# Optimization experiments

Measured on AMD Instinct MI355X. Metric: run time of the kernel, lower is better.

## Reference

```python
import jax, jax.numpy as jnp
import numpy as np

N, NS, D, HID = 8192, 512, 1024, 1024  # nodes, num_edges, f_dim, mlp hidden (max(f_dim,128))


def layernorm(x, g, b, eps=1e-5):
    m = x.mean(-1, keepdims=True)
    v = x.var(-1, keepdims=True)
    return (x - m) / jnp.sqrt(v + eps) * g + b


def mask_topk(a, kk):
    # keep only the top-kk entries of each row (vectorized version of mask_attn)
    _, idx = jax.lax.top_k(a, kk)
    rows = jnp.arange(a.shape[0])[:, None]
    mask = jnp.zeros(a.shape, a.dtype).at[rows, idx].set(1.0)
    return a * mask


def setup_inputs() -> dict:
    key = jax.random.key(0)
    ks = jax.random.split(key, 16)
    xavier = lambda k, i, o: jax.random.uniform(k, (i, o), jnp.float32, -1.0, 1.0) * np.sqrt(6.0 / (i + o))
    return {
        "inputs": jax.random.normal(ks[0], (N, D), jnp.float32),
        "noise": jax.random.normal(ks[1], (NS, D), jnp.float32),
        "edges_mu": jax.random.normal(ks[2], (1, D), jnp.float32),
        "edges_logsigma": xavier(ks[3], 1, D),
        "Wq": xavier(ks[4], D, D), "bq": jnp.zeros((D,), jnp.float32),
        "Wk": xavier(ks[5], D, D), "bk": jnp.zeros((D,), jnp.float32),
        "Wv": xavier(ks[6], D, D), "bv": jnp.zeros((D,), jnp.float32),
        "W1": xavier(ks[7], 2 * D, HID), "b1": jnp.zeros((HID,), jnp.float32),
        "W2": xavier(ks[8], HID, D), "b2": jnp.zeros((D,), jnp.float32),
        "g_in": jnp.ones((D,), jnp.float32), "b_in": jnp.zeros((D,), jnp.float32),
        "g_e": jnp.ones((D,), jnp.float32), "b_e": jnp.zeros((D,), jnp.float32),
        "k_n": 64,
        "k_e": 8,
    }


def reference(inputs, noise, edges_mu, edges_logsigma, Wq, bq, Wk, bk, Wv, bv,
              W1, b1, W2, b2, g_in, b_in, g_e, b_e, k_n, k_e):
    n, d = inputs.shape
    scale = d ** -0.5
    eps = 1e-8
    x = layernorm(inputs, g_in, b_in)                       # norm_input
    k = jax.nn.relu(x @ Wk + bk)                            # [N, D]
    v = jax.nn.relu(x @ Wv + bv)                            # [N, D]
    edges = edges_mu + jnp.exp(edges_logsigma) * noise      # [NS, D]
    # single iteration (iters=1)
    edges = layernorm(edges, g_e, b_e)                      # norm_edgs
    q = jax.nn.relu(edges @ Wq + bq)                        # [NS, D]
    dots = jnp.einsum('ni,mi->nm', q, k) * scale            # [NS, N]
    attn = jax.nn.softmax(dots, axis=1) + eps
    attn = attn / attn.sum(axis=1, keepdims=True)
    attn = mask_topk(attn, k_n)
    updates = jnp.einsum('nm,md->nd', attn, v)              # [NS, D]
    edges = jnp.concatenate([edges, updates], axis=1)       # [NS, 2D]
    edges = jax.nn.relu(edges @ W1 + b1) @ W2 + b2          # mlp -> [NS, D]
    q2 = x @ Wq + bq                                        # no relu in source
    k2 = jax.nn.relu(edges @ Wk + bk)                       # [NS, D]
    dots_v = jnp.einsum('ni,mi->nm', q2, k2) * scale        # [N, NS]
    attn_v = jax.nn.softmax(dots_v, axis=1)
    H = mask_topk(attn_v, k_e)
    return edges, H, dots
```

## Files before the change

kernel.cpp:

```cpp
#include <hip/hip_runtime.h>
#include <stdint.h>
#include <stddef.h>

typedef unsigned short u16;
typedef __bf16 bf16x8 __attribute__((ext_vector_type(8)));
typedef float f32x4 __attribute__((ext_vector_type(4)));

#define DEV __device__ __forceinline__

DEV float bf2f(u16 u){ union{uint32_t i; float f;} c; c.i=(uint32_t)u<<16; return c.f; }
DEV u16 f2bf(float f){ union{float f; uint32_t i;} c; c.f=f; uint32_t x=c.i;
  uint32_t r = x + 0x7FFFu + ((x>>16)&1u); return (u16)(r>>16); }
DEV uint32_t fmap(float f){ union{float f; uint32_t u;} c; c.f=f;
  return (c.u & 0x80000000u) ? ~c.u : (c.u | 0x80000000u); }
DEV float funmap(uint32_t u){ union{uint32_t u; float f;} c;
  c.u = (u & 0x80000000u) ? (u & 0x7FFFFFFFu) : ~u; return c.f; }
DEV void split2(float x, u16& h, u16& l){ h = f2bf(x); l = f2bf(x - bf2f(h)); }

DEV void xcd_swizzle(int& bx, int& by){
  const int gx = gridDim.x, nwg = gx * gridDim.y;
  const int b  = blockIdx.x + gx*blockIdx.y;
  const int sb = (b & 7)*(nwg >> 3) + (b >> 3);
  bx = sb % gx; by = sb / gx;
}

DEV float bredsum(float v, float* buf, int tid){
  #pragma unroll
  for(int o=32;o;o>>=1) v += __shfl_down(v,o);
  __syncthreads();
  if((tid&63)==0) buf[tid>>6]=v;
  __syncthreads();
  return buf[0]+buf[1]+buf[2]+buf[3];
}
DEV float bredmax(float v, float* buf, int tid){
  #pragma unroll
  for(int o=32;o;o>>=1) v = fmaxf(v, __shfl_down(v,o));
  __syncthreads();
  if((tid&63)==0) buf[tid>>6]=v;
  __syncthreads();
  return fmaxf(fmaxf(buf[0],buf[1]),fmaxf(buf[2],buf[3]));
}
DEV int bredsumi(int v, int* buf, int tid){
  #pragma unroll
  for(int o=32;o;o>>=1) v += __shfl_down(v,o);
  __syncthreads();
  if((tid&63)==0) buf[tid>>6]=v;
  __syncthreads();
  return buf[0]+buf[1]+buf[2]+buf[3];
}

template<bool RELU, int SK>
__global__ __launch_bounds__(256)
void gemm1_64(const u16* __restrict__ A, int lda,
              const u16* __restrict__ Bt, int ldb,
              const float* __restrict__ bias, float scale,
              u16* __restrict__ outb, float* __restrict__ outf,
              float* __restrict__ part,
              int K, int ldc, int M)
{
  __shared__ __align__(16) u16 As[64*32];
  __shared__ __align__(16) u16 Bs[128*32];
  const int tid = threadIdx.x, lane = tid&63, wave = tid>>6;
  const int m0 = blockIdx.y*64, n0 = blockIdx.x*128;
  const int wm = (wave>>1)*32, wn = (wave&1)*64;
  const int ml = lane&15, quad = lane>>4;
  const int ks = K / SK;
  const int kbeg = blockIdx.z * ks;
  const u16* pa  = A  + (size_t)(m0+(tid>>2))*lda + kbeg + (tid&3)*8;
  const u16* pb0 = Bt + (size_t)(n0+(tid>>2))*ldb + kbeg + (tid&3)*8;
  const u16* pb1 = Bt + (size_t)(n0+64+(tid>>2))*ldb + kbeg + (tid&3)*8;

  f32x4 acc[2][4];
  #pragma unroll
  for(int i=0;i<2;i++)
    #pragma unroll
    for(int j=0;j<4;j++) acc[i][j] = (f32x4){0.f,0.f,0.f,0.f};

  uint4 ra=*(const uint4*)pa, rb0=*(const uint4*)pb0, rb1=*(const uint4*)pb1;
  for(int k0=0;k0<ks;k0+=32){
    __syncthreads();
    *(uint4*)&As[tid*8]       = ra;
    *(uint4*)&Bs[tid*8]       = rb0;
    *(uint4*)&Bs[(256+tid)*8] = rb1;
    __syncthreads();
    if(k0+32<ks){
      ra  = *(const uint4*)(pa +k0+32);
      rb0 = *(const uint4*)(pb0+k0+32);
      rb1 = *(const uint4*)(pb1+k0+32);
    }
    bf16x8 af[2], bf[4];
    #pragma unroll
    for(int mi=0;mi<2;mi++) af[mi] = *(const bf16x8*)&As[(wm+mi*16+ml)*32 + quad*8];
    #pragma unroll
    for(int ni=0;ni<4;ni++) bf[ni] = *(const bf16x8*)&Bs[(wn+ni*16+ml)*32 + quad*8];
    #pragma unroll
    for(int mi=0;mi<2;mi++)
      #pragma unroll
      for(int ni=0;ni<4;ni++)
        acc[mi][ni] = __builtin_amdgcn_mfma_f32_16x16x32_bf16(af[mi], bf[ni], acc[mi][ni], 0,0,0);
  }
  #pragma unroll
  for(int mi=0;mi<2;mi++){
    const int rbase = m0 + wm + mi*16 + quad*4;
    #pragma unroll
    for(int ni=0;ni<4;ni++){
      const int col = n0 + wn + ni*16 + ml;
      if(SK==1){
        const float bv = bias ? bias[col] : 0.f;
        #pragma unroll
        for(int r=0;r<4;r++){
          float v = acc[mi][ni][r]*scale + bv;
          if(RELU) v = fmaxf(v, 0.f);
          const size_t idx = (size_t)(rbase + r)*ldc + col;
          if(outb) outb[idx] = f2bf(v);
          if(outf) outf[idx] = v;
        }
      }else{
        #pragma unroll
        for(int r=0;r<4;r++)
          part[((size_t)blockIdx.z*M + rbase + r)*ldc + col] = acc[mi][ni][r];
      }
    }
  }
}

template<bool RELU>
__global__ __launch_bounds__(256)
void gemm1_128(const u16* __restrict__ A, int lda,
               const u16* __restrict__ Bt, int ldb,
               const float* __restrict__ bias, float scale,
               u16* __restrict__ outb, float* __restrict__ outf,
               int K, int ldc)
{
  __shared__ __align__(16) u16 As[128*32];
  __shared__ __align__(16) u16 Bs[128*32];
  const int tid = threadIdx.x, lane = tid&63, wave = tid>>6;
  int bxs, bys; xcd_swizzle(bxs, bys);
  const int m0 = bys*128, n0 = bxs*128;
  const int wm = (wave>>1)*64, wn = (wave&1)*64;
  const int ml = lane&15, quad = lane>>4;
  const u16* pa0 = A  + (size_t)(m0+(tid>>2))*lda    + (tid&3)*8;
  const u16* pa1 = A  + (size_t)(m0+64+(tid>>2))*lda + (tid&3)*8;
  const u16* pb0 = Bt + (size_t)(n0+(tid>>2))*ldb    + (tid&3)*8;
  const u16* pb1 = Bt + (size_t)(n0+64+(tid>>2))*ldb + (tid&3)*8;

  f32x4 acc[4][4];
  #pragma unroll
  for(int i=0;i<4;i++)
    #pragma unroll
    for(int j=0;j<4;j++) acc[i][j] = (f32x4){0.f,0.f,0.f,0.f};

  uint4 ra0=*(const uint4*)pa0, ra1=*(const uint4*)pa1;
  uint4 rb0=*(const uint4*)pb0, rb1=*(const uint4*)pb1;
  for(int k0=0;k0<K;k0+=32){
    __syncthreads();
    *(uint4*)&As[tid*8]       = ra0;
    *(uint4*)&As[(256+tid)*8] = ra1;
    *(uint4*)&Bs[tid*8]       = rb0;
    *(uint4*)&Bs[(256+tid)*8] = rb1;
    __syncthreads();
    if(k0+32<K){
      ra0 = *(const uint4*)(pa0+k0+32);
      ra1 = *(const uint4*)(pa1+k0+32);
      rb0 = *(const uint4*)(pb0+k0+32);
      rb1 = *(const uint4*)(pb1+k0+32);
    }
    bf16x8 af[4], bf[4];
    #pragma unroll
    for(int mi=0;mi<4;mi++) af[mi] = *(const bf16x8*)&As[(wm+mi*16+ml)*32 + quad*8];
    #pragma unroll
    for(int ni=0;ni<4;ni++) bf[ni] = *(const bf16x8*)&Bs[(wn+ni*16+ml)*32 + quad*8];
    #pragma unroll
    for(int mi=0;mi<4;mi++)
      #pragma unroll
      for(int ni=0;ni<4;ni++)
        acc[mi][ni] = __builtin_amdgcn_mfma_f32_16x16x32_bf16(af[mi], bf[ni], acc[mi][ni], 0,0,0);
  }
  #pragma unroll
  for(int mi=0;mi<4;mi++){
    const int rbase = m0 + wm + mi*16 + quad*4;
    #pragma unroll
    for(int ni=0;ni<4;ni++){
      const int col = n0 + wn + ni*16 + ml;
      const float bv = bias ? bias[col] : 0.f;
      #pragma unroll
      for(int r=0;r<4;r++){
        float v = acc[mi][ni][r]*scale + bv;
        if(RELU) v = fmaxf(v, 0.f);
        const size_t idx = (size_t)(rbase + r)*ldc + col;
        if(outb) outb[idx] = f2bf(v);
        if(outf) outf[idx] = v;
      }
    }
  }
}

__global__ __launch_bounds__(256)
void gemm_kv_128(const u16* __restrict__ A, int lda,
                 const u16* __restrict__ Bt, int ldb,
                 const float* __restrict__ bk, const float* __restrict__ bv,
                 u16* __restrict__ kb, u16* __restrict__ vb, int K)
{
  __shared__ __align__(16) u16 As[128*32];
  __shared__ __align__(16) u16 Bs[128*32];
  const int tid = threadIdx.x, lane = tid&63, wave = tid>>6;
  int bxs, bys; xcd_swizzle(bxs, bys);
  const int m0 = bys*128, n0 = bxs*128;
  const int wm = (wave>>1)*64, wn = (wave&1)*64;
  const int ml = lane&15, quad = lane>>4;
  const u16* pa0 = A  + (size_t)(m0+(tid>>2))*lda    + (tid&3)*8;
  const u16* pa1 = A  + (size_t)(m0+64+(tid>>2))*lda + (tid&3)*8;
  const u16* pb0 = Bt + (size_t)(n0+(tid>>2))*ldb    + (tid&3)*8;
  const u16* pb1 = Bt + (size_t)(n0+64+(tid>>2))*ldb + (tid&3)*8;

  f32x4 acc[4][4];
  #pragma unroll
  for(int i=0;i<4;i++)
    #pragma unroll
    for(int j=0;j<4;j++) acc[i][j] = (f32x4){0.f,0.f,0.f,0.f};

  uint4 ra0=*(const uint4*)pa0, ra1=*(const uint4*)pa1;
  uint4 rb0=*(const uint4*)pb0, rb1=*(const uint4*)pb1;
  for(int k0=0;k0<K;k0+=32){
    __syncthreads();
    *(uint4*)&As[tid*8]       = ra0;
    *(uint4*)&As[(256+tid)*8] = ra1;
    *(uint4*)&Bs[tid*8]       = rb0;
    *(uint4*)&Bs[(256+tid)*8] = rb1;
    __syncthreads();
    if(k0+32<K){
      ra0 = *(const uint4*)(pa0+k0+32);
      ra1 = *(const uint4*)(pa1+k0+32);
      rb0 = *(const uint4*)(pb0+k0+32);
      rb1 = *(const uint4*)(pb1+k0+32);
    }
    bf16x8 af[4], bf[4];
    #pragma unroll
    for(int mi=0;mi<4;mi++) af[mi] = *(const bf16x8*)&As[(wm+mi*16+ml)*32 + quad*8];
    #pragma unroll
    for(int ni=0;ni<4;ni++) bf[ni] = *(const bf16x8*)&Bs[(wn+ni*16+ml)*32 + quad*8];
    #pragma unroll
    for(int mi=0;mi<4;mi++)
      #pragma unroll
      for(int ni=0;ni<4;ni++)
        acc[mi][ni] = __builtin_amdgcn_mfma_f32_16x16x32_bf16(af[mi], bf[ni], acc[mi][ni], 0,0,0);
  }
  #pragma unroll
  for(int mi=0;mi<4;mi++){
    const int rbase = m0 + wm + mi*16 + quad*4;
    #pragma unroll
    for(int ni=0;ni<4;ni++){
      const int col = n0 + wn + ni*16 + ml;
      const bool isv = col >= 1024;
      const int c2 = col & 1023;
      const float bb = isv ? bv[c2] : bk[c2];
      u16* outp = isv ? vb : kb;
      #pragma unroll
      for(int r=0;r<4;r++){
        const float v = fmaxf(acc[mi][ni][r] + bb, 0.f);
        outp[(size_t)(rbase + r)*1024 + c2] = f2bf(v);
      }
    }
  }
}

template<bool RELU, int SK>
__global__ __launch_bounds__(256)
void gemm3_64(const u16* __restrict__ Ah, const u16* __restrict__ Al, int lda,
              const u16* __restrict__ Bh, const u16* __restrict__ Bl, int ldb,
              const float* __restrict__ bias, float scale,
              u16* __restrict__ outh, u16* __restrict__ outl,
              float* __restrict__ outf, float* __restrict__ part,
              int K, int ldc, int M)
{
  __shared__ __align__(16) u16 AsH[64*32];
  __shared__ __align__(16) u16 AsL[64*32];
  __shared__ __align__(16) u16 BsH[128*32];
  __shared__ __align__(16) u16 BsL[128*32];
  const int tid = threadIdx.x, lane = tid&63, wave = tid>>6;
  const int m0 = blockIdx.y*64, n0 = blockIdx.x*128;
  const int wm = (wave>>1)*32, wn = (wave&1)*64;
  const int ml = lane&15, quad = lane>>4;
  const int ks = K / SK;
  const int kbeg = blockIdx.z * ks;
  const size_t ao  = (size_t)(m0+(tid>>2))*lda + kbeg + (tid&3)*8;
  const size_t bo0 = (size_t)(n0+(tid>>2))*ldb + kbeg + (tid&3)*8;
  const size_t bo1 = (size_t)(n0+64+(tid>>2))*ldb + kbeg + (tid&3)*8;

  f32x4 acc[2][4];
  #pragma unroll
  for(int i=0;i<2;i++)
    #pragma unroll
    for(int j=0;j<4;j++) acc[i][j] = (f32x4){0.f,0.f,0.f,0.f};

  uint4 rah=*(const uint4*)(Ah+ao),  ral=*(const uint4*)(Al+ao);
  uint4 rbh0=*(const uint4*)(Bh+bo0), rbl0=*(const uint4*)(Bl+bo0);
  uint4 rbh1=*(const uint4*)(Bh+bo1), rbl1=*(const uint4*)(Bl+bo1);
  for(int k0=0;k0<ks;k0+=32){
    __syncthreads();
    *(uint4*)&AsH[tid*8]       = rah;
    *(uint4*)&AsL[tid*8]       = ral;
    *(uint4*)&BsH[tid*8]       = rbh0;
    *(uint4*)&BsL[tid*8]       = rbl0;
    *(uint4*)&BsH[(256+tid)*8] = rbh1;
    *(uint4*)&BsL[(256+tid)*8] = rbl1;
    __syncthreads();
    if(k0+32<ks){
      const int s = k0+32;
      rah =*(const uint4*)(Ah+ao +s); ral =*(const uint4*)(Al+ao +s);
      rbh0=*(const uint4*)(Bh+bo0+s); rbl0=*(const uint4*)(Bl+bo0+s);
      rbh1=*(const uint4*)(Bh+bo1+s); rbl1=*(const uint4*)(Bl+bo1+s);
    }
    bf16x8 afh[2], afl[2], bfh[4], bfl[4];
    #pragma unroll
    for(int mi=0;mi<2;mi++){
      const int o = (wm+mi*16+ml)*32 + quad*8;
      afh[mi] = *(const bf16x8*)&AsH[o];
      afl[mi] = *(const bf16x8*)&AsL[o];
    }
    #pragma unroll
    for(int ni=0;ni<4;ni++){
      const int o = (wn+ni*16+ml)*32 + quad*8;
      bfh[ni] = *(const bf16x8*)&BsH[o];
      bfl[ni] = *(const bf16x8*)&BsL[o];
    }
    #pragma unroll
    for(int mi=0;mi<2;mi++)
      #pragma unroll
      for(int ni=0;ni<4;ni++){
        acc[mi][ni] = __builtin_amdgcn_mfma_f32_16x16x32_bf16(afh[mi], bfh[ni], acc[mi][ni], 0,0,0);
        acc[mi][ni] = __builtin_amdgcn_mfma_f32_16x16x32_bf16(afh[mi], bfl[ni], acc[mi][ni], 0,0,0);
        acc[mi][ni] = __builtin_amdgcn_mfma_f32_16x16x32_bf16(afl[mi], bfh[ni], acc[mi][ni], 0,0,0);
      }
  }
  #pragma unroll
  for(int mi=0;mi<2;mi++){
    const int rbase = m0 + wm + mi*16 + quad*4;
    #pragma unroll
    for(int ni=0;ni<4;ni++){
      const int col = n0 + wn + ni*16 + ml;
      if(SK==1){
        const float bv = bias ? bias[col] : 0.f;
        #pragma unroll
        for(int r=0;r<4;r++){
          float v = acc[mi][ni][r]*scale + bv;
          if(RELU) v = fmaxf(v, 0.f);
          const size_t idx = (size_t)(rbase + r)*ldc + col;
          if(outh){ u16 h, l; split2(v, h, l); outh[idx] = h; outl[idx] = l; }
          if(outf) outf[idx] = v;
        }
      }else{
        #pragma unroll
        for(int r=0;r<4;r++)
          part[((size_t)blockIdx.z*M + rbase + r)*ldc + col] = acc[mi][ni][r];
      }
    }
  }
}

__global__ __launch_bounds__(256)
void gemm3_128(const u16* __restrict__ Ah, const u16* __restrict__ Al, int lda,
               const u16* __restrict__ Bh, const u16* __restrict__ Bl, int ldb,
               const float* __restrict__ bias, float scale,
               float* __restrict__ outf, int K, int ldc)
{
  __shared__ __align__(16) u16 AsH[128*32];
  __shared__ __align__(16) u16 AsL[128*32];
  __shared__ __align__(16) u16 BsH[128*32];
  __shared__ __align__(16) u16 BsL[128*32];
  const int tid = threadIdx.x, lane = tid&63, wave = tid>>6;
  int bxs, bys; xcd_swizzle(bxs, bys);
  const int m0 = bys*128, n0 = bxs*128;
  const int wm = (wave>>1)*64, wn = (wave&1)*64;
  const int ml = lane&15, quad = lane>>4;
  const size_t ao0 = (size_t)(m0+(tid>>2))*lda    + (tid&3)*8;
  const size_t ao1 = (size_t)(m0+64+(tid>>2))*lda + (tid&3)*8;
  const size_t bo0 = (size_t)(n0+(tid>>2))*ldb    + (tid&3)*8;
  const size_t bo1 = (size_t)(n0+64+(tid>>2))*ldb + (tid&3)*8;

  f32x4 acc[4][4];
  #pragma unroll
  for(int i=0;i<4;i++)
    #pragma unroll
    for(int j=0;j<4;j++) acc[i][j] = (f32x4){0.f,0.f,0.f,0.f};

  uint4 rah0=*(const uint4*)(Ah+ao0), ral0=*(const uint4*)(Al+ao0);
  uint4 rah1=*(const uint4*)(Ah+ao1), ral1=*(const uint4*)(Al+ao1);
  uint4 rbh0=*(const uint4*)(Bh+bo0), rbl0=*(const uint4*)(Bl+bo0);
  uint4 rbh1=*(const uint4*)(Bh+bo1), rbl1=*(const uint4*)(Bl+bo1);
  for(int k0=0;k0<K;k0+=32){
    __syncthreads();
    *(uint4*)&AsH[tid*8]       = rah0;
    *(uint4*)&AsH[(256+tid)*8] = rah1;
    *(uint4*)&AsL[tid*8]       = ral0;
    *(uint4*)&AsL[(256+tid)*8] = ral1;
    *(uint4*)&BsH[tid*8]       = rbh0;
    *(uint4*)&BsH[(256+tid)*8] = rbh1;
    *(uint4*)&BsL[tid*8]       = rbl0;
    *(uint4*)&BsL[(256+tid)*8] = rbl1;
    __syncthreads();
    if(k0+32<K){
      const int s = k0+32;
      rah0=*(const uint4*)(Ah+ao0+s); ral0=*(const uint4*)(Al+ao0+s);
      rah1=*(const uint4*)(Ah+ao1+s); ral1=*(const uint4*)(Al+ao1+s);
      rbh0=*(const uint4*)(Bh+bo0+s); rbl0=*(const uint4*)(Bl+bo0+s);
      rbh1=*(const uint4*)(Bh+bo1+s); rbl1=*(const uint4*)(Bl+bo1+s);
    }
    bf16x8 afh[4], afl[4], bfh[4], bfl[4];
    #pragma unroll
    for(int mi=0;mi<4;mi++){
      const int o = (wm+mi*16+ml)*32 + quad*8;
      afh[mi] = *(const bf16x8*)&AsH[o];
      afl[mi] = *(const bf16x8*)&AsL[o];
    }
    #pragma unroll
    for(int ni=0;ni<4;ni++){
      const int o = (wn+ni*16+ml)*32 + quad*8;
      bfh[ni] = *(const bf16x8*)&BsH[o];
      bfl[ni] = *(const bf16x8*)&BsL[o];
    }
    #pragma unroll
    for(int mi=0;mi<4;mi++)
      #pragma unroll
      for(int ni=0;ni<4;ni++){
        acc[mi][ni] = __builtin_amdgcn_mfma_f32_16x16x32_bf16(afh[mi], bfh[ni], acc[mi][ni], 0,0,0);
        acc[mi][ni] = __builtin_amdgcn_mfma_f32_16x16x32_bf16(afh[mi], bfl[ni], acc[mi][ni], 0,0,0);
        acc[mi][ni] = __builtin_amdgcn_mfma_f32_16x16x32_bf16(afl[mi], bfh[ni], acc[mi][ni], 0,0,0);
      }
  }
  #pragma unroll
  for(int mi=0;mi<4;mi++){
    const int rbase = m0 + wm + mi*16 + quad*4;
    #pragma unroll
    for(int ni=0;ni<4;ni++){
      const int col = n0 + wn + ni*16 + ml;
      const float bv = bias ? bias[col] : 0.f;
      #pragma unroll
      for(int r=0;r<4;r++){
        const float v = acc[mi][ni][r]*scale + bv;
        outf[(size_t)(rbase + r)*ldc + col] = v;
      }
    }
  }
}

template<bool RELU, int SK>
__global__ __launch_bounds__(256)
void reduce_epi(const float* __restrict__ part, const float* __restrict__ bias,
                float scale, u16* __restrict__ outh, u16* __restrict__ outl,
                u16* __restrict__ outb, float* __restrict__ outf,
                size_t MN, int N,
                const float* __restrict__ bqv, float* __restrict__ bvout)
{
  __shared__ float buf[4];
  const int tid = threadIdx.x;
  const size_t i = ((size_t)blockIdx.x*256 + tid)*4;
  float4 s = *(const float4*)(part + i);
  #pragma unroll
  for(int z=1; z<SK; z++){
    const float4 t = *(const float4*)(part + (size_t)z*MN + i);
    s.x += t.x; s.y += t.y; s.z += t.z; s.w += t.w;
  }
  const int col = (int)(i % (size_t)N);
  float4 bv = bias ? *(const float4*)(bias + col) : (float4){0.f,0.f,0.f,0.f};
  float v[4] = { s.x*scale + bv.x, s.y*scale + bv.y, s.z*scale + bv.z, s.w*scale + bv.w };
  if(RELU){
    #pragma unroll
    for(int j=0;j<4;j++) v[j] = fmaxf(v[j], 0.f);
  }
  if(outh){
    ushort4 h4, l4;
    split2(v[0], h4.x, l4.x); split2(v[1], h4.y, l4.y);
    split2(v[2], h4.z, l4.z); split2(v[3], h4.w, l4.w);
    *(ushort4*)(outh + i) = h4;
    *(ushort4*)(outl + i) = l4;
  }
  if(outb){
    ushort4 b4;
    b4.x=f2bf(v[0]); b4.y=f2bf(v[1]); b4.z=f2bf(v[2]); b4.w=f2bf(v[3]);
    *(ushort4*)(outb + i) = b4;
  }
  if(outf) *(float4*)(outf + i) = (float4){v[0],v[1],v[2],v[3]};
  if(bvout){
    const float4 q = *(const float4*)(bqv + col);
    float d = q.x*v[0] + q.y*v[1] + q.z*v[2] + q.w*v[3];
    d = bredsum(d, buf, tid);
    if(tid==0) bvout[blockIdx.x] = d * 0.03125f;
  }
}

DEV void dev_tsplit(const float* in, u16* oh, u16* ol, int R, int C,
                    int bx, int by, int tid, float (*tile)[33])
{
  const int tx = tid & 31, ty = tid >> 5;
  #pragma unroll
  for(int i=0;i<32;i+=8)
    tile[ty+i][tx] = in[(size_t)(by*32+ty+i)*C + bx*32 + tx];
  __syncthreads();
  #pragma unroll
  for(int i=0;i<32;i+=8){
    const float v = tile[tx][ty+i];
    u16 h, l; split2(v, h, l);
    const size_t o = (size_t)(bx*32+ty+i)*R + by*32 + tx;
    oh[o] = h; if(ol) ol[o] = l;
  }
}
__global__ __launch_bounds__(256)
void prep_weights(const float* __restrict__ Wk, const float* __restrict__ W1,
                  const float* __restrict__ W2, const float* __restrict__ Wv,
                  const float* __restrict__ Wq,
                  u16* __restrict__ WkvTh, u16* __restrict__ WkTl,
                  u16* __restrict__ W1Th,  u16* __restrict__ W1Tl,
                  u16* __restrict__ W2Th,  u16* __restrict__ W2Tl,
                  u16* __restrict__ WqTh,
                  u16* __restrict__ Wqh,   u16* __restrict__ Wql)
{
  __shared__ float tile[32][33];
  const int id = blockIdx.x, tid = threadIdx.x;
  if(id < 1024){
    dev_tsplit(Wk, WkvTh, WkTl, 1024, 1024, id&31, id>>5, tid, tile);
  }else if(id < 3072){
    const int l = id - 1024;
    dev_tsplit(W1, W1Th, W1Tl, 2048, 1024, l&31, l>>5, tid, tile);
  }else if(id < 4096){
    const int l = id - 3072;
    dev_tsplit(W2, W2Th, W2Tl, 1024, 1024, l&31, l>>5, tid, tile);
  }else if(id < 5120){
    const int l = id - 4096;
    dev_tsplit(Wv, WkvTh + 1024*1024, nullptr, 1024, 1024, l&31, l>>5, tid, tile);
  }else if(id < 6144){
    const int l = id - 5120;
    dev_tsplit(Wq, WqTh, nullptr, 1024, 1024, l&31, l>>5, tid, tile);
  }else{
    const int l = id - 6144;
    const int i = l*256 + tid;
    const float4 v = ((const float4*)Wq)[i];
    ushort4 h4, l4;
    split2(v.x, h4.x, l4.x); split2(v.y, h4.y, l4.y);
    split2(v.z, h4.z, l4.z); split2(v.w, h4.w, l4.w);
    ((ushort4*)Wqh)[i] = h4; ((ushort4*)Wql)[i] = l4;
  }
}

__global__ __launch_bounds__(256)
void ln_all(const float* __restrict__ in, const float* __restrict__ g,
            const float* __restrict__ bb, u16* __restrict__ outh,
            u16* __restrict__ outl,
            const float* __restrict__ noise, const float* __restrict__ mu,
            const float* __restrict__ lsig, const float* __restrict__ ge,
            const float* __restrict__ be, u16* __restrict__ cath,
            u16* __restrict__ catl)
{
  __shared__ float buf[4];
  const int tid = threadIdx.x;
  const bool edge = blockIdx.x >= 8192;
  const int row = edge ? (blockIdx.x - 8192) : blockIdx.x;
  float v0,v1,v2,v3;
  if(!edge){
    const float4 xv = ((const float4*)(in + (size_t)row*1024))[tid];
    v0=xv.x; v1=xv.y; v2=xv.z; v3=xv.w;
  }else{
    const float4 nv  = ((const float4*)(noise + (size_t)row*1024))[tid];
    const float4 muv = ((const float4*)mu)[tid];
    const float4 lsv = ((const float4*)lsig)[tid];
    v0 = muv.x + expf(lsv.x)*nv.x;
    v1 = muv.y + expf(lsv.y)*nv.y;
    v2 = muv.z + expf(lsv.z)*nv.z;
    v3 = muv.w + expf(lsv.w)*nv.w;
  }
  float s  = bredsum(v0+v1+v2+v3, buf, tid);
  float s2 = bredsum(v0*v0+v1*v1+v2*v2+v3*v3, buf, tid);
  const float mean = s * (1.f/1024.f);
  const float var  = s2 * (1.f/1024.f) - mean*mean;
  const float rs   = 1.f / sqrtf(var + 1e-5f);
  const float4 gv = ((const float4*)(edge?ge:g))[tid];
  const float4 bv = ((const float4*)(edge?be:bb))[tid];
  float o0 = (v0-mean)*rs*gv.x + bv.x;
  float o1 = (v1-mean)*rs*gv.y + bv.y;
  float o2 = (v2-mean)*rs*gv.z + bv.z;
  float o3 = (v3-mean)*rs*gv.w + bv.w;
  ushort4 oh, ol;
  split2(o0, oh.x, ol.x); split2(o1, oh.y, ol.y);
  split2(o2, oh.z, ol.z); split2(o3, oh.w, ol.w);
  u16* ph = edge ? cath : outh;
  u16* pl = edge ? catl : outl;
  const int ostride = edge ? 2048 : 1024;
  ((ushort4*)(ph + (size_t)row*ostride))[tid] = oh;
  ((ushort4*)(pl + (size_t)row*ostride))[tid] = ol;
}

#define SWZ(i) ((i) ^ (((((unsigned)(i))>>5)&7u)<<2))
__global__ __launch_bounds__(256)
void softmax_topk_a(const float* __restrict__ dots, const int* __restrict__ knp,
                    int* __restrict__ tidx, float* __restrict__ tw)
{
  const int NC = 8192;
  __shared__ __align__(16) uint32_t us[8192];
  __shared__ float fbuf[4];
  __shared__ int ibuf[4];
  __shared__ int scan[256];
  __shared__ uint32_t hist[256];
  __shared__ uint32_t bcast;
  __shared__ int slot_ctr;
  const int row = blockIdx.x, tid = threadIdx.x;
  const int lane = tid & 63, wave = tid >> 6;
  const float* x = dots + (size_t)row * NC;

  float mx = -3.4e38f;
  #pragma unroll
  for(int it=0; it<8; ++it){
    const int i = (tid + it*256)*4;
    const float4 f = *(const float4*)(x + i);
    mx = fmaxf(fmaxf(mx, fmaxf(f.x,f.y)), fmaxf(f.z,f.w));
    uint4 u; u.x=fmap(f.x); u.y=fmap(f.y); u.z=fmap(f.z); u.w=fmap(f.w);
    *(uint4*)&us[SWZ(i)] = u;
  }
  mx = bredmax(mx, fbuf, tid);

  float se = 0.f;
  #pragma unroll
  for(int it=0; it<8; ++it){
    const int i = (tid + it*256)*4;
    const uint4 u = *(const uint4*)&us[SWZ(i)];
    se += expf(funmap(u.x)-mx) + expf(funmap(u.y)-mx)
        + expf(funmap(u.z)-mx) + expf(funmap(u.w)-mx);
  }
  se = bredsum(se, fbuf, tid);
  const float T = 1.f + (float)NC * 1e-8f;

  const int k = knp[0];
  const int base = tid*32;

  uint32_t prefix = 0;
  int remaining = k;
  #pragma unroll
  for(int shift=24; shift>=0; shift-=8){
    hist[tid] = 0;
    __syncthreads();
    const uint32_t himask = (shift==24) ? 0u : (0xFFFFFFFFu << (shift+8));
    #pragma unroll
    for(int j=0;j<32;j+=4){
      const uint4 u4 = *(const uint4*)&us[SWZ(base+j)];
      const uint32_t uu[4] = {u4.x,u4.y,u4.z,u4.w};
      #pragma unroll
      for(int t=0;t<4;t++)
        if((uu[t] & himask) == prefix) atomicAdd(&hist[(uu[t]>>shift)&255u], 1u);
    }
    __syncthreads();
    if(wave==0){
      const uint32_t h0=hist[4*lane], h1=hist[4*lane+1],
                     h2=hist[4*lane+2], h3=hist[4*lane+3];
      const uint32_t s3=h3, s2=h2+s3, s1=h1+s2, s0=h0+s1;
      uint32_t tsum = s0;
      #pragma unroll
      for(int o=1;o<64;o<<=1){
        const uint32_t vv = __shfl_down(tsum, o);
        if(lane + o < 64) tsum += vv;
      }
      const uint32_t excl = tsum - s0;
      const uint32_t r = (uint32_t)remaining;
      int cand = -1; uint32_t gsel = 0;
      if     (s3+excl >= r){ cand = 4*lane+3; gsel = excl; }
      else if(s2+excl >= r){ cand = 4*lane+2; gsel = s3+excl; }
      else if(s1+excl >= r){ cand = 4*lane+1; gsel = s2+excl; }
      else if(s0+excl >= r){ cand = 4*lane+0; gsel = s1+excl; }
      int bestc = cand; uint32_t bestg = gsel;
      #pragma unroll
      for(int o=32;o;o>>=1){
        const int oc = __shfl_xor(bestc, o);
        const uint32_t og = __shfl_xor(bestg, o);
        if(oc > bestc){ bestc = oc; bestg = og; }
      }
      if(lane==0) bcast = (uint32_t)bestc;
      remaining -= (int)bestg;
    }
    __syncthreads();
    prefix |= bcast << shift;
  }
  const uint32_t uth = prefix;

  int gt = 0, eq = 0;
  #pragma unroll
  for(int j=0;j<32;j+=4){
    const uint4 u4 = *(const uint4*)&us[SWZ(base+j)];
    gt += (u4.x>uth)+(u4.y>uth)+(u4.z>uth)+(u4.w>uth);
    eq += (u4.x==uth)+(u4.y==uth)+(u4.z==uth)+(u4.w==uth);
  }
  const int c1 = bredsumi(gt, ibuf, tid);
  __syncthreads();
  scan[tid] = eq;
  __syncthreads();
  #pragma unroll
  for(int o=1;o<256;o<<=1){
    int t = (tid>=o) ? scan[tid-o] : 0;
    __syncthreads();
    scan[tid] += t;
    __syncthreads();
  }
  int eq_rank = scan[tid] - eq;
  const int budget = k - c1;
  if(tid==0) slot_ctr = 0;
  __syncthreads();
  #pragma unroll 2
  for(int j=0;j<32;j+=4){
    const uint4 u4 = *(const uint4*)&us[SWZ(base+j)];
    const uint32_t uu[4] = {u4.x,u4.y,u4.z,u4.w};
    #pragma unroll
    for(int t=0;t<4;t++){
      const uint32_t u = uu[t];
      bool sel = (u > uth);
      if(u == uth){ sel = (eq_rank < budget); eq_rank++; }
      if(sel){
        const int s = atomicAdd(&slot_ctr, 1);
        const float f = funmap(u);
        const float w = (expf(f - mx)/se + 1e-8f) / T;
        if(s < 128){ tidx[row*128 + s] = base + j + t; tw[row*128 + s] = w; }
      }
    }
  }
}

__global__ __launch_bounds__(256)
void gather_updates(const int* __restrict__ tidx, const float* __restrict__ tw,
                    const int* __restrict__ knp, const u16* __restrict__ v,
                    u16* __restrict__ cath, u16* __restrict__ catl)
{
  __shared__ int   idx_s[128];
  __shared__ float w_s[128];
  const int row = blockIdx.x, tid = threadIdx.x;
  const int kk = knp[0];
  if(tid < 128){
    idx_s[tid] = (tid < kk) ? (tidx[row*128+tid] & 8191) : 0;
    w_s[tid]   = (tid < kk) ? tw[row*128+tid] : 0.f;
  }
  __syncthreads();
  const int c = tid*4;
  float a0=0,a1=0,a2=0,a3=0;
  for(int j=0;j<kk && j<128;j++){
    const ushort4 vv = *(const ushort4*)&v[(size_t)idx_s[j]*1024 + c];
    const float w = w_s[j];
    a0 += w*bf2f(vv.x); a1 += w*bf2f(vv.y); a2 += w*bf2f(vv.z); a3 += w*bf2f(vv.w);
  }
  ushort4 oh, ol;
  split2(a0, oh.x, ol.x); split2(a1, oh.y, ol.y);
  split2(a2, oh.z, ol.z); split2(a3, oh.w, ol.w);
  ((ushort4*)(cath + (size_t)row*2048 + 1024))[tid] = oh;
  ((ushort4*)(catl + (size_t)row*2048 + 1024))[tid] = ol;
}

__global__ __launch_bounds__(256)
void softmax_topk_h_wave(const float* __restrict__ dv, const int* __restrict__ kep,
                         float* __restrict__ H)
{
  const int wave = threadIdx.x >> 6, lane = threadIdx.x & 63;
  const int row = blockIdx.x*4 + wave;
  const float* x = dv + (size_t)row*512 + lane*8;
  const float4 a = *(const float4*)x;
  const float4 b = *(const float4*)(x+4);
  float vals[8] = {a.x,a.y,a.z,a.w,b.x,b.y,b.z,b.w};

  float mx = vals[0];
  #pragma unroll
  for(int j=1;j<8;j++) mx = fmaxf(mx, vals[j]);
  #pragma unroll
  for(int o=32;o;o>>=1) mx = fmaxf(mx, __shfl_xor(mx, o));
  float e[8], se = 0.f;
  #pragma unroll
  for(int j=0;j<8;j++){ e[j] = expf(vals[j]-mx); se += e[j]; }
  #pragma unroll
  for(int o=32;o;o>>=1) se += __shfl_xor(se, o);
  const float inv = 1.f/se;

  const int k = kep[0];
  unsigned int selmask = 0;
  for(int r=0;r<k;r++){
    unsigned long long best = 0;
    #pragma unroll
    for(int j=0;j<8;j++){
      if(!((selmask>>j)&1u)){
        const unsigned long long key =
          ((unsigned long long)fmap(vals[j]) << 9) | (unsigned long long)(511 - (lane*8+j));
        if(key > best) best = key;
      }
    }
    #pragma unroll
    for(int o=32;o;o>>=1){
      const unsigned long long other = __shfl_xor(best, o);
      if(other > best) best = other;
    }
    const int bidx = 511 - (int)(best & 511ull);
    if((bidx>>3) == lane) selmask |= 1u << (bidx & 7);
  }

  float4 o0, o1;
  o0.x = (selmask&  1u) ? e[0]*inv : 0.f;
  o0.y = (selmask&  2u) ? e[1]*inv : 0.f;
  o0.z = (selmask&  4u) ? e[2]*inv : 0.f;
  o0.w = (selmask&  8u) ? e[3]*inv : 0.f;
  o1.x = (selmask& 16u) ? e[4]*inv : 0.f;
  o1.y = (selmask& 32u) ? e[5]*inv : 0.f;
  o1.z = (selmask& 64u) ? e[6]*inv : 0.f;
  o1.w = (selmask&128u) ? e[7]*inv : 0.f;
  float* outp = H + (size_t)row*512 + lane*8;
  *(float4*)outp     = o0;
  *(float4*)(outp+4) = o1;
}

extern "C" void kernel_launch(void* const* d_in, const int* in_sizes, int n_in,
                              void* d_out, int out_size, void* d_ws, size_t ws_size,
                              hipStream_t stream)
{
  const float* inputs = (const float*)d_in[0];
  const float* noise  = (const float*)d_in[1];
  const float* emu    = (const float*)d_in[2];
  const float* elsig  = (const float*)d_in[3];
  const float* Wq = (const float*)d_in[4];  const float* bq = (const float*)d_in[5];
  const float* Wk = (const float*)d_in[6];  const float* bk = (const float*)d_in[7];
  const float* Wv = (const float*)d_in[8];  const float* bv = (const float*)d_in[9];
  const float* W1 = (const float*)d_in[10]; const float* b1 = (const float*)d_in[11];
  const float* W2 = (const float*)d_in[12]; const float* b2 = (const float*)d_in[13];
  const float* g_in = (const float*)d_in[14]; const float* b_in = (const float*)d_in[15];
  const float* g_e  = (const float*)d_in[16]; const float* b_e  = (const float*)d_in[17];
  const int* knp = (const int*)d_in[18];
  const int* kep = (const int*)d_in[19];

  float* out = (float*)d_out;
  float* out_edges = out;
  float* out_H     = out + 512*1024;
  float* out_dots  = out + 512*1024 + 8192*512;

  char* p = (char*)d_ws;
  const size_t MB = 1024ull*1024;
  u16* xh = (u16*)(p + 0*MB);
  u16* xl = (u16*)(p + 16*MB);
  u16* kb = (u16*)(p + 32*MB);
  u16* vb = (u16*)(p + 48*MB);
  float* dotsvf = (float*)(p + 32*MB);
  u16* WkvTh = (u16*)(p + 64*MB);
  u16* WkTl  = (u16*)(p + 68*MB);
  u16* WqTh  = (u16*)(p + 70*MB);
  u16* Wqh   = (u16*)(p + 72*MB);  u16* Wql  = (u16*)(p + 74*MB);
  u16* W1Th  = (u16*)(p + 76*MB);  u16* W1Tl = (u16*)(p + 80*MB);
  u16* W2Th  = (u16*)(p + 84*MB);  u16* W2Tl = (u16*)(p + 86*MB);
  u16* cath = (u16*)(p + 88*MB);  u16* catl = (u16*)(p + 90*MB);
  u16* qmb  = (u16*)(p + 92*MB);
  u16* h1h  = (u16*)(p + 93*MB);  u16* h1l  = (u16*)(p + 94*MB);
  u16* eoh  = (u16*)(p + 95*MB);  u16* eol  = (u16*)(p + 96*MB);
  u16* k2h  = (u16*)(p + 97*MB);  u16* k2l  = (u16*)(p + 98*MB);
  u16* Gth  = (u16*)(p + 99*MB);  u16* Gtl  = (u16*)(p + 100*MB);
  int*   tidx  = (int*)  (p + 101*MB);
  float* tw    = (float*)(p + 101*MB + 256*1024);
  float* biasv = (float*)(p + 101*MB + 512*1024);
  float* part  = (float*)(p + 104*MB);

  hipMemsetAsync(tidx, 0, 512ull*128*4*2, stream);

  prep_weights<<<7168,256,0,stream>>>(Wk, W1, W2, Wv, Wq,
                                      WkvTh, WkTl, W1Th, W1Tl, W2Th, W2Tl,
                                      WqTh, Wqh, Wql);
  ln_all<<<8704,256,0,stream>>>(inputs, g_in, b_in, xh, xl,
                                noise, emu, elsig, g_e, b_e, cath, catl);

  const size_t MN = 512ull*1024;
  gemm_kv_128<<<dim3(16,64),256,0,stream>>>(xh,1024, WkvTh,1024, bk, bv,
                                            kb, vb, 1024);
  gemm1_64<false,4><<<dim3(8,8,4),256,0,stream>>>(cath,2048, WqTh,1024, nullptr, 1.f,
                                                  nullptr,nullptr, part, 1024,1024,512);
  reduce_epi<true,4><<<512,256,0,stream>>>(part, bq, 1.f, nullptr,nullptr, qmb,nullptr,
                                           MN, 1024, nullptr, nullptr);
  gemm1_128<false><<<dim3(64,4),256,0,stream>>>(qmb,1024, kb,1024, nullptr, 0.03125f,
                                                nullptr,out_dots, 1024,8192);
  softmax_topk_a<<<512,256,0,stream>>>(out_dots, knp, tidx, tw);
  gather_updates<<<512,256,0,stream>>>(tidx, tw, knp, vb, cath, catl);

  gemm3_64<false,4><<<dim3(8,8,4),256,0,stream>>>(cath,catl,2048, W1Th,W1Tl,2048,
                                                  nullptr,1.f, nullptr,nullptr,nullptr,
                                                  part, 2048,1024,512);
  reduce_epi<true,4><<<512,256,0,stream>>>(part, b1, 1.f, h1h,h1l, nullptr,nullptr,
                                           MN, 1024, nullptr, nullptr);
  gemm3_64<false,4><<<dim3(8,8,4),256,0,stream>>>(h1h,h1l,1024, W2Th,W2Tl,1024,
                                                  nullptr,1.f, nullptr,nullptr,nullptr,
                                                  part, 1024,1024,512);
  reduce_epi<false,4><<<512,256,0,stream>>>(part, b2, 1.f, eoh,eol, nullptr,out_edges,
                                            MN, 1024, nullptr, nullptr);
  gemm3_64<false,4><<<dim3(8,8,4),256,0,stream>>>(eoh,eol,1024, WkvTh,WkTl,1024,
                                                  nullptr,1.f, nullptr,nullptr,nullptr,
                                                  part, 1024,1024,512);
  reduce_epi<true,4><<<512,256,0,stream>>>(part, bk, 1.f, k2h,k2l, nullptr,nullptr,
                                           MN, 1024, bq, biasv);
  gemm3_64<false,4><<<dim3(8,8,4),256,0,stream>>>(k2h,k2l,1024, Wqh,Wql,1024,
                                                  nullptr,1.f, nullptr,nullptr,nullptr,
                                                  part, 1024,1024,512);
  reduce_epi<false,4><<<512,256,0,stream>>>(part, nullptr, 1.f, Gth,Gtl, nullptr,nullptr,
                                            MN, 1024, nullptr, nullptr);
  gemm3_128<<<dim3(4,64),256,0,stream>>>(xh,xl,1024, Gth,Gtl,1024,
                                         biasv, 0.03125f, dotsvf, 1024,512);
  softmax_topk_h_wave<<<2048,256,0,stream>>>(dotsvf, kep, out_H);
}
```

Measured before the change: 383.8 us.

## Use 256x256 tiles with 4-stage direct-to-LDS async pipeline in KV GEMM

Rewrites the fused K/V projection GEMM to use 256x256 tiles with 512 threads and a four-stage LDS ring buffer. Tiles are filled by global_load_lds direct-to-LDS loads, with vmcnt waits replacing register staging. The aim is to hide global load latency and raise data reuse per block, at the cost of more LDS and accumulator registers per block. Also drops the memset of the top-k index buffer, which assumes later kernels fully overwrite it.

```diff
diff --git a/kernel.cpp b/kernel.cpp
--- a/kernel.cpp
+++ b/kernel.cpp
@@ -3,10 +3,15 @@
 #include <stddef.h>
 
 typedef unsigned short u16;
+typedef uint32_t u32;
 typedef __bf16 bf16x8 __attribute__((ext_vector_type(8)));
 typedef float f32x4 __attribute__((ext_vector_type(4)));
 
 #define DEV __device__ __forceinline__
+
+#define GLD16(g, l) __builtin_amdgcn_global_load_lds( \
+    (const __attribute__((address_space(1))) u32*)(g), \
+    (__attribute__((address_space(3))) u32*)(l), 16, 0, 0)
 
 DEV float bf2f(u16 u){ union{uint32_t i; float f;} c; c.i=(uint32_t)u<<16; return c.f; }
 DEV u16 f2bf(float f){ union{float f; uint32_t i;} c; c.f=f; uint32_t x=c.i;
@@ -195,62 +200,70 @@
   }
 }
 
-__global__ __launch_bounds__(256)
-void gemm_kv_128(const u16* __restrict__ A, int lda,
+__global__ __launch_bounds__(512)
+void gemm_kv_256(const u16* __restrict__ A, int lda,
                  const u16* __restrict__ Bt, int ldb,
                  const float* __restrict__ bk, const float* __restrict__ bv,
                  u16* __restrict__ kb, u16* __restrict__ vb, int K)
 {
-  __shared__ __align__(16) u16 As[128*32];
-  __shared__ __align__(16) u16 Bs[128*32];
+  __shared__ __align__(16) u16 As[4][256*32];
+  __shared__ __align__(16) u16 Bs[4][256*32];
   const int tid = threadIdx.x, lane = tid&63, wave = tid>>6;
   int bxs, bys; xcd_swizzle(bxs, bys);
-  const int m0 = bys*128, n0 = bxs*128;
-  const int wm = (wave>>1)*64, wn = (wave&1)*64;
+  const int m0 = bys*256, n0 = bxs*256;
+  const int wmw = (wave>>2)*128, wnw = (wave&3)*64;
   const int ml = lane&15, quad = lane>>4;
-  const u16* pa0 = A  + (size_t)(m0+(tid>>2))*lda    + (tid&3)*8;
-  const u16* pa1 = A  + (size_t)(m0+64+(tid>>2))*lda + (tid&3)*8;
-  const u16* pb0 = Bt + (size_t)(n0+(tid>>2))*ldb    + (tid&3)*8;
-  const u16* pb1 = Bt + (size_t)(n0+64+(tid>>2))*ldb + (tid&3)*8;
-
-  f32x4 acc[4][4];
-  #pragma unroll
-  for(int i=0;i<4;i++)
+  const int r0 = tid>>2,        c0 = (tid&3)*8;
+  const int r1 = (tid+512)>>2,  c1 = ((tid+512)&3)*8;
+  const u16* pa0 = A  + (size_t)(m0+r0)*lda + c0;
+  const u16* pa1 = A  + (size_t)(m0+r1)*lda + c1;
+  const u16* pb0 = Bt + (size_t)(n0+r0)*ldb + c0;
+  const u16* pb1 = Bt + (size_t)(n0+r1)*ldb + c1;
+  const int d0 = r0*32 + c0, d1 = r1*32 + c1;
+
+  f32x4 acc[8][4];
+  #pragma unroll
+  for(int i=0;i<8;i++)
     #pragma unroll
     for(int j=0;j<4;j++) acc[i][j] = (f32x4){0.f,0.f,0.f,0.f};
 
-  uint4 ra0=*(const uint4*)pa0, ra1=*(const uint4*)pa1;
-  uint4 rb0=*(const uint4*)pb0, rb1=*(const uint4*)pb1;
-  for(int k0=0;k0<K;k0+=32){
-    __syncthreads();
-    *(uint4*)&As[tid*8]       = ra0;
-    *(uint4*)&As[(256+tid)*8] = ra1;
-    *(uint4*)&Bs[tid*8]       = rb0;
-    *(uint4*)&Bs[(256+tid)*8] = rb1;
-    __syncthreads();
-    if(k0+32<K){
-      ra0 = *(const uint4*)(pa0+k0+32);
-      ra1 = *(const uint4*)(pa1+k0+32);
-      rb0 = *(const uint4*)(pb0+k0+32);
-      rb1 = *(const uint4*)(pb1+k0+32);
-    }
-    bf16x8 af[4], bf[4];
-    #pragma unroll
-    for(int mi=0;mi<4;mi++) af[mi] = *(const bf16x8*)&As[(wm+mi*16+ml)*32 + quad*8];
-    #pragma unroll
-    for(int ni=0;ni<4;ni++) bf[ni] = *(const bf16x8*)&Bs[(wn+ni*16+ml)*32 + quad*8];
-    #pragma unroll
-    for(int mi=0;mi<4;mi++)
+  #define KV_STAGE(t, s) do{                    \
+    GLD16(pa0 + (t)*32, &As[s][d0]);            \
+    GLD16(pa1 + (t)*32, &As[s][d1]);            \
+    GLD16(pb0 + (t)*32, &Bs[s][d0]);            \
+    GLD16(pb1 + (t)*32, &Bs[s][d1]); }while(0)
+
+  KV_STAGE(0,0); KV_STAGE(1,1); KV_STAGE(2,2);
+  const int NT = K >> 5;
+  for(int t=0;t<NT;t++){
+    if(t+3<NT) KV_STAGE(t+3, (t+3)&3);
+    const int rem = NT-1-t;
+    if(rem>=3)      asm volatile("s_waitcnt vmcnt(12)" ::: "memory");
+    else if(rem==2) asm volatile("s_waitcnt vmcnt(8)"  ::: "memory");
+    else if(rem==1) asm volatile("s_waitcnt vmcnt(4)"  ::: "memory");
+    else            asm volatile("s_waitcnt vmcnt(0)"  ::: "memory");
+    __builtin_amdgcn_s_barrier();
+    const int s = t&3;
+    bf16x8 af[8], bf[4];
+    #pragma unroll
+    for(int mi=0;mi<8;mi++) af[mi] = *(const bf16x8*)&As[s][(wmw+mi*16+ml)*32 + quad*8];
+    #pragma unroll
+    for(int ni=0;ni<4;ni++) bf[ni] = *(const bf16x8*)&Bs[s][(wnw+ni*16+ml)*32 + quad*8];
+    #pragma unroll
+    for(int mi=0;mi<8;mi++)
       #pragma unroll
       for(int ni=0;ni<4;ni++)
         acc[mi][ni] = __builtin_amdgcn_mfma_f32_16x16x32_bf16(af[mi], bf[ni], acc[mi][ni], 0,0,0);
-  }
-  #pragma unroll
-  for(int mi=0;mi<4;mi++){
-    const int rbase = m0 + wm + mi*16 + quad*4;
+    __builtin_amdgcn_s_barrier();
+  }
+  #undef KV_STAGE
+
+  #pragma unroll
+  for(int mi=0;mi<8;mi++){
+    const int rbase = m0 + wmw + mi*16 + quad*4;
     #pragma unroll
     for(int ni=0;ni<4;ni++){
-      const int col = n0 + wn + ni*16 + ml;
+      const int col = n0 + wnw + ni*16 + ml;
       const bool isv = col >= 1024;
       const int c2 = col & 1023;
       const float bb = isv ? bv[c2] : bk[c2];
@@ -853,7 +866,6 @@
   float* biasv = (float*)(p + 101*MB + 512*1024);
   float* part  = (float*)(p + 104*MB);
 
-  hipMemsetAsync(tidx, 0, 512ull*128*4*2, stream);
 
   prep_weights<<<7168,256,0,stream>>>(Wk, W1, W2, Wv, Wq,
                                       WkvTh, WkTl, W1Th, W1Tl, W2Th, W2Tl,
@@ -862,8 +874,8 @@
                                 noise, emu, elsig, g_e, b_e, cath, catl);
 
   const size_t MN = 512ull*1024;
-  gemm_kv_128<<<dim3(16,64),256,0,stream>>>(xh,1024, WkvTh,1024, bk, bv,
-                                            kb, vb, 1024);
+  gemm_kv_256<<<dim3(8,32),512,0,stream>>>(xh,1024, WkvTh,1024, bk, bv,
+                                           kb, vb, 1024);
   gemm1_64<false,4><<<dim3(8,8,4),256,0,stream>>>(cath,2048, WqTh,1024, nullptr, 1.f,
                                                   nullptr,nullptr, part, 1024,1024,512);
   reduce_epi<true,4><<<512,256,0,stream>>>(part, bq, 1.f, nullptr,nullptr, qmb,nullptr,
```

New measurement: 378.7 us. About the same (-1.3%).
